# Kernel optimization log

Measured on AMD Instinct MI355X. Metric: run time of the kernel, lower is better.

The kernel has to match this reference:

```python
import jax, jax.numpy as jnp
import numpy as np

A_BITS = 16
W_BITS = 8
KH = KW = 3
STRIDE = 1
PADDING = 1


def fake_quant(x, bits, axes=None):
    """Asymmetric min/max fake quantization with straight-through estimator."""
    if axes is None:
        mn = x.min()
        mx = x.max()
    else:
        mn = x.min(axis=axes, keepdims=True)
        mx = x.max(axis=axes, keepdims=True)
    qmax = float(2 ** bits - 1)
    scale = jnp.maximum((mx - mn) / qmax, 1e-12)
    zp = jnp.round(-mn / scale)
    q = jnp.clip(jnp.round(x / scale) + zp, 0.0, qmax)
    deq = (q - zp) * scale
    # STE: identity gradient through the quantizer
    return x + jax.lax.stop_gradient(deq - x)


def unfold(x, kh, kw, stride, padding):
    """torch.nn.functional.unfold equivalent -> (N, C*kh*kw, Hout*Wout)."""
    N, C, H, W = x.shape
    xp = jnp.pad(x, ((0, 0), (0, 0), (padding, padding), (padding, padding)))
    Ho = (H - kh + 2 * padding) // stride + 1
    Wo = (W - kw + 2 * padding) // stride + 1
    cols = []
    for i in range(kh):          # small fixed 3x3 loop
        for j in range(kw):
            cols.append(xp[:, :, i:i + Ho * stride:stride, j:j + Wo * stride:stride])
    xcol = jnp.stack(cols, axis=2)              # (N, C, kh*kw, Ho, Wo)
    return xcol.reshape(N, C * kh * kw, Ho * Wo), Ho, Wo


def adder_op(W_col, X_col):
    # W_col: (F, K), X_col: (K, L) -> out: (F, L); L1-distance "conv"
    return -jnp.abs(W_col[:, :, None] - X_col[None, :, :]).sum(axis=1)


def setup_inputs() -> dict:
    key = jax.random.key(0)
    kx, kw = jax.random.split(key)
    x = jax.random.normal(kx, (4, 64, 28, 28), dtype=jnp.float32)
    W = jax.random.normal(kw, (64, 64, 3, 3), dtype=jnp.float32)
    return {"x": x, "W": W}


def reference(x, W):
    # first_layer == 0 -> activation fake-quant; per-channel weight fake-quant
    qx = fake_quant(x, A_BITS)
    qw = fake_quant(W, W_BITS, axes=(1, 2, 3))
    N = x.shape[0]
    F = W.shape[0]
    xcol, Ho, Wo = unfold(qx, KH, KW, STRIDE, PADDING)   # (N, K, L0)
    K = xcol.shape[1]
    # torch: permute(1,2,0).view(K, L0*N) -> batch fastest within a row
    X_col = jnp.transpose(xcol, (1, 2, 0)).reshape(K, -1)  # (K, L0*N)
    W_col = qw.reshape(F, K)
    out = adder_op(W_col, X_col)                            # (F, L0*N)
    out = out.reshape(F, Ho, Wo, N).transpose(3, 0, 1, 2)   # (N, F, Ho, Wo)
    return out
```

## Files before the change

### kernel.cpp

```cpp
#include <hip/hip_runtime.h>
#include <math.h>

#define N_  4
#define C_  64
#define H_  28
#define W_  28
#define F_  64
#define KK  576
#define NX  (N_*C_*H_*W_)
#define NX4 (NX/4)


__global__ __launch_bounds__(256) void k_prep(const float* __restrict__ x,
                                              const float* __restrict__ Wg,
                                              float* __restrict__ ws) {
  __shared__ float sm[4], sM[4];
  int tid = threadIdx.x, lane = tid & 63, wv = tid >> 6;

  const float4* x4 = (const float4*)x;
  float m = 3.4e38f, M = -3.4e38f;
  for (int i = blockIdx.x * 256 + tid; i < NX4; i += 64 * 256) {
    float4 v = x4[i];
    m = fminf(m, fminf(fminf(v.x, v.y), fminf(v.z, v.w)));
    M = fmaxf(M, fmaxf(fmaxf(v.x, v.y), fmaxf(v.z, v.w)));
  }
  #pragma unroll
  for (int o = 32; o; o >>= 1) {
    m = fminf(m, __shfl_xor(m, o));
    M = fmaxf(M, __shfl_xor(M, o));
  }
  if (lane == 0) { sm[wv] = m; sM[wv] = M; }
  __syncthreads();
  if (tid == 0) {
    m = fminf(fminf(sm[0], sm[1]), fminf(sm[2], sm[3]));
    M = fmaxf(fmaxf(sM[0], sM[1]), fmaxf(sM[2], sM[3]));
    ws[blockIdx.x] = m;
    ws[64 + blockIdx.x] = M;
  }

  if (blockIdx.x < 16) {
    int f = blockIdx.x * 4 + wv;
    const float* wp = Wg + f * KK;
    float v[9];
    float wm = 3.4e38f, wM = -3.4e38f;
    #pragma unroll
    for (int u = 0; u < 9; ++u) {
      v[u] = wp[lane + 64 * u];
      wm = fminf(wm, v[u]);
      wM = fmaxf(wM, v[u]);
    }
    #pragma unroll
    for (int o = 32; o; o >>= 1) {
      wm = fminf(wm, __shfl_xor(wm, o));
      wM = fmaxf(wM, __shfl_xor(wM, o));
    }
    float s = fmaxf((wM - wm) / 255.0f, 1e-12f);
    float z = rintf(-wm / s);
    float rs = 1.0f / s;
    float* Wt = ws + 256;
    #pragma unroll
    for (int u = 0; u < 9; ++u) {
      float q = fminf(fmaxf(rintf(v[u] * rs) + z, 0.0f), 255.0f);
      Wt[(lane + 64 * u) * 64 + f] = (q - z) * s;
    }
  }
}

__global__ __launch_bounds__(256) void k_main(const float* __restrict__ x,
                                              const float* __restrict__ ws,
                                              float* __restrict__ out) {
  __shared__ __align__(16) float Xs[64 * 3 * 32];
  __shared__ __align__(16) float Wl[KK * 33];
  int tid  = threadIdx.x;
  int lane = tid & 63;
  int y = blockIdx.x, n = blockIdx.y, fh = blockIdx.z;

  float m = ws[lane], M = ws[64 + lane];
  #pragma unroll
  for (int o = 32; o; o >>= 1) {
    m = fminf(m, __shfl_xor(m, o));
    M = fmaxf(M, __shfl_xor(M, o));
  }
  float sx = fmaxf((M - m) / 65535.0f, 1e-12f);
  float zx = rintf(-m / sx);
  float rx = 1.0f / sx;

  for (int idx = tid; idx < 64 * 3 * 30; idx += 256) {
    int c = idx / 90, rem = idx - c * 90;
    int r = rem / 30, p = rem - r * 30;
    int row = y + r - 1, col = p - 1;
    float v = 0.0f;
    if ((unsigned)row < 28u && (unsigned)col < 28u) {
      float raw = x[((n * 64 + c) * 28 + row) * 28 + col];
      float q = fminf(fmaxf(rintf(raw * rx) + zx, 0.0f), 65535.0f);
      v = (q - zx) * sx;
    }
    Xs[(c * 3 + r) * 32 + p] = v;
  }

  {
    const float4* Wt4 = (const float4*)(ws + 256);
    #pragma unroll
    for (int i = 0; i < 18; ++i) {
      int idx = tid + 256 * i;
      int k = idx >> 3, q = idx & 7;
      float4 v = Wt4[k * 16 + fh * 8 + q];
      float* d = &Wl[k * 33 + q * 4];
      d[0] = v.x; d[1] = v.y; d[2] = v.z; d[3] = v.w;
    }
  }

  __syncthreads();

  int fl = tid & 31, g = tid >> 5;
  int base = g * 4;
  bool active = (base < 28);
  float acc0 = 0.f, acc1 = 0.f, acc2 = 0.f, acc3 = 0.f;

  if (active) {
    const float* xb = &Xs[base];
    const float* wb = &Wl[fl];
    #pragma unroll 2
    for (int c = 0; c < 64; ++c) {
      const float* xr = xb + c * 96;
      float4 a0 = *(const float4*)(xr);
      float4 a1 = *(const float4*)(xr + 4);
      float4 b0 = *(const float4*)(xr + 32);
      float4 b1 = *(const float4*)(xr + 36);
      float4 c0 = *(const float4*)(xr + 64);
      float4 c1 = *(const float4*)(xr + 68);
      const float* wr = wb + c * 297;
      float w0 = wr[0],   w1 = wr[33],  w2 = wr[66];
      float w3 = wr[99],  w4 = wr[132], w5 = wr[165];
      float w6 = wr[198], w7 = wr[231], w8 = wr[264];

      acc0 += fabsf(w0 - a0.x) + fabsf(w1 - a0.y) + fabsf(w2 - a0.z)
            + fabsf(w3 - b0.x) + fabsf(w4 - b0.y) + fabsf(w5 - b0.z)
            + fabsf(w6 - c0.x) + fabsf(w7 - c0.y) + fabsf(w8 - c0.z);
      acc1 += fabsf(w0 - a0.y) + fabsf(w1 - a0.z) + fabsf(w2 - a0.w)
            + fabsf(w3 - b0.y) + fabsf(w4 - b0.z) + fabsf(w5 - b0.w)
            + fabsf(w6 - c0.y) + fabsf(w7 - c0.z) + fabsf(w8 - c0.w);
      acc2 += fabsf(w0 - a0.z) + fabsf(w1 - a0.w) + fabsf(w2 - a1.x)
            + fabsf(w3 - b0.z) + fabsf(w4 - b0.w) + fabsf(w5 - b1.x)
            + fabsf(w6 - c0.z) + fabsf(w7 - c0.w) + fabsf(w8 - c1.x);
      acc3 += fabsf(w0 - a0.w) + fabsf(w1 - a1.x) + fabsf(w2 - a1.y)
            + fabsf(w3 - b0.w) + fabsf(w4 - b1.x) + fabsf(w5 - b1.y)
            + fabsf(w6 - c0.w) + fabsf(w7 - c1.x) + fabsf(w8 - c1.y);
    }
    int f = fh * 32 + fl;
    float4* o = (float4*)(out + ((n * 64 + f) * 28 + y) * 28 + base);
    *o = make_float4(-acc0, -acc1, -acc2, -acc3);
  }
}

extern "C" void kernel_launch(void* const* d_in, const int* in_sizes, int n_in,
                              void* d_out, int out_size, void* d_ws, size_t ws_size,
                              hipStream_t stream) {
  const float* x  = (const float*)d_in[0];
  const float* Wg = (const float*)d_in[1];
  float* out = (float*)d_out;
  float* ws  = (float*)d_ws;

  hipLaunchKernelGGL(k_prep, dim3(64), dim3(256), 0, stream, x, Wg, ws);
  hipLaunchKernelGGL(k_main, dim3(28, 4, 2), dim3(256), 0, stream, x, ws, out);
}
```

Before: 85.48 us.

## Split channel reduction across warps with register-held weights and shared-memory reduce

The main kernel no longer stages the weight tile in shared memory. Each thread now keeps one filter's 9 weights in registers, prefetching the next channel's weights from global memory, and computes all 28 output columns for an 8-channel slice. Partial sums from the 8 channel groups are reduced through a shared buffer before the store. Previously only 7 of 8 thread groups were active, so this removes that idle group and the large weight LDS copy. In exchange it needs 28 accumulators per thread, an extra reduction pass with a barrier, and scalar stores instead of float4 stores.

```diff
diff --git a/kernel.cpp b/kernel.cpp
--- a/kernel.cpp
+++ b/kernel.cpp
@@ -66,13 +66,14 @@
   }
 }
 
-__global__ __launch_bounds__(256) void k_main(const float* __restrict__ x,
-                                              const float* __restrict__ ws,
-                                              float* __restrict__ out) {
+__global__ __launch_bounds__(256, 1) void k_main(const float* __restrict__ x,
+                                                 const float* __restrict__ ws,
+                                                 float* __restrict__ out) {
   __shared__ __align__(16) float Xs[64 * 3 * 32];
-  __shared__ __align__(16) float Wl[KK * 33];
-  int tid  = threadIdx.x;
+  __shared__ float Rbuf[8 * 32 * 29];
+  int tid = threadIdx.x;
   int lane = tid & 63;
+  int fl = tid & 31, cq = tid >> 5;
   int y = blockIdx.x, n = blockIdx.y, fh = blockIdx.z;
 
   float m = ws[lane], M = ws[64 + lane];
@@ -97,59 +98,51 @@
     }
     Xs[(c * 3 + r) * 32 + p] = v;
   }
+  __syncthreads();
 
+  const float* Wt = ws + 256;
+  int f = fh * 32 + fl;
+  float acc[28];
+  #pragma unroll
+  for (int i = 0; i < 28; ++i) acc[i] = 0.0f;
+
+  float w[9], wn[9];
   {
-    const float4* Wt4 = (const float4*)(ws + 256);
+    const float* wp = Wt + (cq * 8) * 9 * 64 + f;
     #pragma unroll
-    for (int i = 0; i < 18; ++i) {
-      int idx = tid + 256 * i;
-      int k = idx >> 3, q = idx & 7;
-      float4 v = Wt4[k * 16 + fh * 8 + q];
-      float* d = &Wl[k * 33 + q * 4];
-      d[0] = v.x; d[1] = v.y; d[2] = v.z; d[3] = v.w;
+    for (int k = 0; k < 9; ++k) wn[k] = wp[k * 64];
+  }
+  for (int ci = 0; ci < 8; ++ci) {
+    #pragma unroll
+    for (int k = 0; k < 9; ++k) w[k] = wn[k];
+    if (ci < 7) {
+      const float* wp = Wt + (cq * 8 + ci + 1) * 9 * 64 + f;
+      #pragma unroll
+      for (int k = 0; k < 9; ++k) wn[k] = wp[k * 64];
+    }
+    const float* xr = &Xs[(cq * 8 + ci) * 96];
+    #pragma unroll
+    for (int p = 0; p < 28; ++p) {
+      float s0 = fabsf(w[0] - xr[p])      + fabsf(w[1] - xr[p + 1])  + fabsf(w[2] - xr[p + 2]);
+      float s1 = fabsf(w[3] - xr[32 + p]) + fabsf(w[4] - xr[33 + p]) + fabsf(w[5] - xr[34 + p]);
+      float s2 = fabsf(w[6] - xr[64 + p]) + fabsf(w[7] - xr[65 + p]) + fabsf(w[8] - xr[66 + p]);
+      acc[p] += s0 + s1 + s2;
     }
   }
 
+  #pragma unroll
+  for (int p = 0; p < 28; ++p) Rbuf[(cq * 32 + fl) * 29 + p] = acc[p];
   __syncthreads();
 
-  int fl = tid & 31, g = tid >> 5;
-  int base = g * 4;
-  bool active = (base < 28);
-  float acc0 = 0.f, acc1 = 0.f, acc2 = 0.f, acc3 = 0.f;
-
-  if (active) {
-    const float* xb = &Xs[base];
-    const float* wb = &Wl[fl];
-    #pragma unroll 2
-    for (int c = 0; c < 64; ++c) {
-      const float* xr = xb + c * 96;
-      float4 a0 = *(const float4*)(xr);
-      float4 a1 = *(const float4*)(xr + 4);
-      float4 b0 = *(const float4*)(xr + 32);
-      float4 b1 = *(const float4*)(xr + 36);
-      float4 c0 = *(const float4*)(xr + 64);
-      float4 c1 = *(const float4*)(xr + 68);
-      const float* wr = wb + c * 297;
-      float w0 = wr[0],   w1 = wr[33],  w2 = wr[66];
-      float w3 = wr[99],  w4 = wr[132], w5 = wr[165];
-      float w6 = wr[198], w7 = wr[231], w8 = wr[264];
-
-      acc0 += fabsf(w0 - a0.x) + fabsf(w1 - a0.y) + fabsf(w2 - a0.z)
-            + fabsf(w3 - b0.x) + fabsf(w4 - b0.y) + fabsf(w5 - b0.z)
-            + fabsf(w6 - c0.x) + fabsf(w7 - c0.y) + fabsf(w8 - c0.z);
-      acc1 += fabsf(w0 - a0.y) + fabsf(w1 - a0.z) + fabsf(w2 - a0.w)
-            + fabsf(w3 - b0.y) + fabsf(w4 - b0.z) + fabsf(w5 - b0.w)
-            + fabsf(w6 - c0.y) + fabsf(w7 - c0.z) + fabsf(w8 - c0.w);
-      acc2 += fabsf(w0 - a0.z) + fabsf(w1 - a0.w) + fabsf(w2 - a1.x)
-            + fabsf(w3 - b0.z) + fabsf(w4 - b0.w) + fabsf(w5 - b1.x)
-            + fabsf(w6 - c0.z) + fabsf(w7 - c0.w) + fabsf(w8 - c1.x);
-      acc3 += fabsf(w0 - a0.w) + fabsf(w1 - a1.x) + fabsf(w2 - a1.y)
-            + fabsf(w3 - b0.w) + fabsf(w4 - b1.x) + fabsf(w5 - b1.y)
-            + fabsf(w6 - c0.w) + fabsf(w7 - c1.x) + fabsf(w8 - c1.y);
+  for (int i = 0; i < 4; ++i) {
+    int idx = tid + 256 * i;
+    if (idx < 896) {
+      int ff = idx / 28, col = idx - ff * 28;
+      float s = 0.0f;
+      #pragma unroll
+      for (int q = 0; q < 8; ++q) s += Rbuf[(q * 32 + ff) * 29 + col];
+      out[((n * 64 + fh * 32 + ff) * 28 + y) * 28 + col] = -s;
     }
-    int f = fh * 32 + fl;
-    float4* o = (float4*)(out + ((n * 64 + f) * 28 + y) * 28 + base);
-    *o = make_float4(-acc0, -acc1, -acc2, -acc3);
   }
 }
 
```

New measurement: 82.50 us. 1.04x faster.
